# Kernel optimization log

Hardware: AMD Instinct MI355X
Metric: run time of the kernel (lower is better)

Reference implementation:

```python
import jax, jax.numpy as jnp
import numpy as np

N = 50000      # nodes
E = 800000     # edges
H, C = 4, 32   # heads, per-head channels
NF = 513       # n_fft//2 + 1 frequency bins
NMEL = 128
NEG_SLOPE_ATT = 0.2   # GATConv leaky_relu slope
NEG_SLOPE_MLP = 0.01  # F.leaky_relu default


def setup_inputs() -> dict:
    key = jax.random.key(0)
    ks = jax.random.split(key, 12)
    s = 0.05
    return {
        "x": jax.random.normal(ks[0], (N, NF), jnp.float32),
        "edge_index": jax.random.randint(ks[1], (2, E), 0, N, dtype=jnp.int32),
        "fb": jax.random.normal(ks[2], (NF, NMEL), jnp.float32) * s,
        "Wg": jax.random.normal(ks[3], (NMEL, H * C), jnp.float32) * s,
        "bias_g": jnp.zeros((H * C,), jnp.float32),
        "att_src": jax.random.normal(ks[4], (H, C), jnp.float32) * s,
        "att_dst": jax.random.normal(ks[5], (H, C), jnp.float32) * s,
        "W1": jax.random.normal(ks[6], (H * C, 256), jnp.float32) * s,
        "b1": jnp.zeros((256,), jnp.float32),
        "W2": jax.random.normal(ks[7], (256, 128), jnp.float32) * s,
        "b2": jnp.zeros((128,), jnp.float32),
        "W3": jax.random.normal(ks[8], (128, 10), jnp.float32) * s,
        "b3": jnp.zeros((10,), jnp.float32),
    }


def gat_conv(h, src, dst, att_src, att_dst, bias_g):
    # h: [N, H, C]; per-edge attention, segment softmax over dst, scatter-add
    a_s = jnp.einsum('nhc,hc->nh', h, att_src)  # [N, H]
    a_d = jnp.einsum('nhc,hc->nh', h, att_dst)  # [N, H]
    e = jax.nn.leaky_relu(a_s[src] + a_d[dst], NEG_SLOPE_ATT)  # [E', H]
    m = jax.ops.segment_max(e, dst, num_segments=N)            # [N, H]
    ex = jnp.exp(e - m[dst])
    denom = jax.ops.segment_sum(ex, dst, num_segments=N)       # [N, H]
    alpha = ex / denom[dst]                                    # [E', H]
    msg = h[src] * alpha[:, :, None]                           # [E', H, C]
    out = jax.ops.segment_sum(msg, dst, num_segments=N)        # [N, H, C]
    return out.reshape(N, H * C) + bias_g


def reference(x, edge_index, fb, Wg, bias_g, att_src, att_dst, W1, b1, W2, b2, W3, b3):
    # learnable mel filterbank projection: [N, NF] -> [N, NMEL]
    x = x @ fb
    # GATConv linear transform, split into heads
    h = (x @ Wg).reshape(N, H, C)
    # add self loops (PyG GATConv default add_self_loops=True)
    loop = jnp.arange(N, dtype=edge_index.dtype)
    src = jnp.concatenate([edge_index[0], loop])
    dst = jnp.concatenate([edge_index[1], loop])
    x = jax.nn.elu(gat_conv(h, src, dst, att_src, att_dst, bias_g))
    # dropout is identity in eval mode
    x = jax.nn.leaky_relu(x @ W1 + b1, NEG_SLOPE_MLP)
    x = jax.nn.leaky_relu(x @ W2 + b2, NEG_SLOPE_MLP)
    x = jax.nn.leaky_relu(x @ W3 + b3, NEG_SLOPE_MLP)
    return jax.nn.softmax(x, axis=-1)
```

## Files before the change

kernel.cpp:

```cpp
#include <hip/hip_runtime.h>
#include <hip/hip_bf16.h>

#define NN 50000
#define EE 800000
#define NFR 513
#define NMEL 128
#define HC 128

typedef __bf16 bf16x8 __attribute__((ext_vector_type(8)));
typedef float floatx4 __attribute__((ext_vector_type(4)));

struct __attribute__((packed, aligned(4))) u4a { unsigned x, y, z, w; };

__device__ __forceinline__ unsigned short f2b(float f) {
    unsigned u = __float_as_uint(f);
    u = (u + 0x7FFFu + ((u >> 16) & 1u)) >> 16;
    return (unsigned short)u;
}
__device__ __forceinline__ unsigned short f2bu(unsigned u) {
    u = (u + 0x7FFFu + ((u >> 16) & 1u)) >> 16;
    return (unsigned short)u;
}
__device__ __forceinline__ float b2f(unsigned short s) {
    return __uint_as_float(((unsigned)s) << 16);
}
__device__ __forceinline__ float lexp(float a) {
    a = a > 0.f ? a : 0.2f * a;
    return __expf(a);
}

__device__ __forceinline__ float ldf(const float* p, long i) { return p[i]; }
__device__ __forceinline__ void stf(float* p, long i, float v) { p[i] = v; }
__device__ __forceinline__ void stf(__hip_bfloat16* p, long i, float v) {
    ((unsigned short*)p)[i] = f2b(v);
}

#define BM 64
#define BN 64
#define BK 16

template<int EPI, typename TA, typename TB, typename TC>
__global__ __launch_bounds__(256) void gemm_k(const TA* __restrict__ A, const TB* __restrict__ B,
                                              TC* __restrict__ C, int M, int Nn, int K,
                                              const float* __restrict__ bias)
{
    __shared__ float As[BK][BM + 4];
    __shared__ float Bs[BK][BN + 4];
    const int t = threadIdx.x;
    const int row0 = blockIdx.x * BM;
    const int col0 = blockIdx.y * BN;
    const int tc = t & 15, tr = t >> 4;
    float acc[4][4] = {};

    for (int kb = 0; kb < K; kb += BK) {
        #pragma unroll
        for (int i = 0; i < 4; ++i) {
            int idx = i * 256 + t;
            int r = idx >> 4, k = idx & 15;
            int gr = row0 + r, gk = kb + k;
            float v = 0.f;
            if (gr < M && gk < K) v = ldf(A, (long)gr * K + gk);
            As[k][r] = v;
        }
        #pragma unroll
        for (int i = 0; i < 4; ++i) {
            int idx = i * 256 + t;
            int c = idx & 63, k = idx >> 6;
            int gk = kb + k, gc = col0 + c;
            float v = 0.f;
            if (gk < K && gc < Nn) v = ldf(B, (long)gk * Nn + gc);
            Bs[k][c] = v;
        }
        __syncthreads();
        #pragma unroll
        for (int kk = 0; kk < BK; ++kk) {
            float4 av = *reinterpret_cast<const float4*>(&As[kk][tr << 2]);
            float4 bv = *reinterpret_cast<const float4*>(&Bs[kk][tc << 2]);
            float a[4] = {av.x, av.y, av.z, av.w};
            float b[4] = {bv.x, bv.y, bv.z, bv.w};
            #pragma unroll
            for (int i = 0; i < 4; ++i)
                #pragma unroll
                for (int j = 0; j < 4; ++j)
                    acc[i][j] += a[i] * b[j];
        }
        __syncthreads();
    }

    #pragma unroll
    for (int i = 0; i < 4; ++i) {
        int gr = row0 + (tr << 2) + i;
        if (gr >= M) continue;
        #pragma unroll
        for (int j = 0; j < 4; ++j) {
            int gc = col0 + (tc << 2) + j;
            if (gc >= Nn) continue;
            float v = acc[i][j];
            if (EPI == 2) {
                stf(C, (long)gc * 544 + gr, v);
            } else {
                if (EPI == 1) { v += bias[gc]; v = v > 0.f ? v : 0.01f * v; }
                stf(C, (long)gr * Nn + gc, v);
            }
        }
    }
}

__global__ void k_trans(const float* __restrict__ in, __hip_bfloat16* __restrict__ outp,
                        int K, int N, int KP)
{
    int id = blockIdx.x * 256 + threadIdx.x;
    if (id >= N * KP) return;
    int n = id / KP, k = id % KP;
    float v = (k < K) ? in[(long)k * N + n] : 0.f;
    ((unsigned short*)outp)[id] = f2b(v);
}

#define PS 40

template<typename T> struct ARegs;
template<> struct ARegs<float> { unsigned v[8]; };
template<> struct ARegs<__hip_bfloat16> { uint4 v; };

__device__ __forceinline__ void loadA_r(const float* __restrict__ A, ARegs<float>& r, int t,
                                        int row0, int M, int K, int kb)
{
    #pragma unroll
    for (int g = 0; g < 2; ++g) {
        int q = g * 256 + t;
        int row = q >> 3, k4 = (q & 7) * 4;
        int gr = row0 + row, gk = kb + k4;
        unsigned f0 = 0, f1 = 0, f2 = 0, f3 = 0;
        if (gr < M) {
            const float* ap = A + (long)gr * K + gk;
            if (gk + 3 < K) {
                u4a u = *reinterpret_cast<const u4a*>(ap);
                f0 = u.x; f1 = u.y; f2 = u.z; f3 = u.w;
            } else {
                if (gk + 0 < K) f0 = __float_as_uint(ap[0]);
                if (gk + 1 < K) f1 = __float_as_uint(ap[1]);
                if (gk + 2 < K) f2 = __float_as_uint(ap[2]);
            }
        }
        r.v[g * 4 + 0] = f0; r.v[g * 4 + 1] = f1;
        r.v[g * 4 + 2] = f2; r.v[g * 4 + 3] = f3;
    }
}

__device__ __forceinline__ void writeA_r(unsigned short* As, const ARegs<float>& r, int t)
{
    #pragma unroll
    for (int g = 0; g < 2; ++g) {
        int q = g * 256 + t;
        int row = q >> 3, k4 = (q & 7) * 4;
        ushort4 pk;
        pk.x = f2bu(r.v[g * 4 + 0]); pk.y = f2bu(r.v[g * 4 + 1]);
        pk.z = f2bu(r.v[g * 4 + 2]); pk.w = f2bu(r.v[g * 4 + 3]);
        *reinterpret_cast<ushort4*>(&As[row * PS + k4]) = pk;
    }
}

__device__ __forceinline__ void loadA_r(const __hip_bfloat16* __restrict__ A, ARegs<__hip_bfloat16>& r,
                                        int t, int row0, int M, int K, int kb)
{
    int row = t >> 2, k8 = (t & 3) * 8;
    int gr = row0 + row;
    uint4 val = make_uint4(0, 0, 0, 0);
    if (gr < M) val = *reinterpret_cast<const uint4*>(A + (long)gr * K + kb + k8);
    r.v = val;
}

__device__ __forceinline__ void writeA_r(unsigned short* As, const ARegs<__hip_bfloat16>& r, int t)
{
    int row = t >> 2, k8 = (t & 3) * 8;
    *reinterpret_cast<uint4*>(&As[row * PS + k8]) = r.v;
}

__device__ __forceinline__ void loadB_r(const __hip_bfloat16* __restrict__ Bt, uint4* bR, int t,
                                        int col0, int Nn, int KB, int kb)
{
    #pragma unroll
    for (int g = 0; g < 2; ++g) {
        int c = g * 256 + t;
        int row = c >> 2, k8 = (c & 3) * 8;
        int gn = col0 + row;
        uint4 val = make_uint4(0, 0, 0, 0);
        if (gn < Nn) val = *reinterpret_cast<const uint4*>(Bt + (long)gn * KB + kb + k8);
        bR[g] = val;
    }
}

__device__ __forceinline__ void writeB_r(unsigned short* Bs, const uint4* bR, int t)
{
    #pragma unroll
    for (int g = 0; g < 2; ++g) {
        int c = g * 256 + t;
        int row = c >> 2, k8 = (c & 3) * 8;
        *reinterpret_cast<uint4*>(&Bs[row * PS + k8]) = bR[g];
    }
}

template<int EPI, typename TA, typename TC>
__global__ __launch_bounds__(256) void mgemm(const TA* __restrict__ A,
                                             const __hip_bfloat16* __restrict__ Bt,
                                             TC* __restrict__ C,
                                             int M, int Nn, int K, int KB,
                                             const float* __restrict__ bias,
                                             const float* __restrict__ pf1,
                                             const float* __restrict__ pf2,
                                             float* __restrict__ po1,
                                             float* __restrict__ po2)
{
    __shared__ unsigned short As[2][64 * PS];
    __shared__ unsigned short Bs[2][128 * PS];

    const int t = threadIdx.x;
    const int row0 = blockIdx.x * 64;
    const int col0 = blockIdx.y * 128;
    const int wave = t >> 6, lane = t & 63;
    const int wm = (wave >> 1) * 32, wn = (wave & 1) * 64;
    const int lm = lane & 15, kq = lane >> 4;

    floatx4 acc[2][4];
    #pragma unroll
    for (int i = 0; i < 2; ++i)
        #pragma unroll
        for (int j = 0; j < 4; ++j)
            acc[i][j] = 0.f;

    ARegs<TA> aR;
    uint4 bR[2];
    loadA_r(A, aR, t, row0, M, K, 0);
    loadB_r(Bt, bR, t, col0, Nn, KB, 0);

    const int nIter = KB >> 5;
    int b = 0;
    for (int it = 0; it < nIter; ++it) {
        writeA_r(As[b], aR, t);
        writeB_r(Bs[b], bR, t);
        if (it + 1 < nIter) {
            loadA_r(A, aR, t, row0, M, K, (it + 1) * 32);
            loadB_r(Bt, bR, t, col0, Nn, KB, (it + 1) * 32);
        }
        asm volatile("s_waitcnt lgkmcnt(0)" ::: "memory");
        __builtin_amdgcn_s_barrier();
        __builtin_amdgcn_sched_barrier(0);

        bf16x8 af[2], bf[4];
        #pragma unroll
        for (int i = 0; i < 2; ++i)
            af[i] = *reinterpret_cast<const bf16x8*>(&As[b][(wm + i * 16 + lm) * PS + kq * 8]);
        #pragma unroll
        for (int j = 0; j < 4; ++j)
            bf[j] = *reinterpret_cast<const bf16x8*>(&Bs[b][(wn + j * 16 + lm) * PS + kq * 8]);
        #pragma unroll
        for (int i = 0; i < 2; ++i)
            #pragma unroll
            for (int j = 0; j < 4; ++j)
                acc[i][j] = __builtin_amdgcn_mfma_f32_16x16x32_bf16(af[i], bf[j], acc[i][j], 0, 0, 0);
        b ^= 1;
    }

    #pragma unroll
    for (int i = 0; i < 2; ++i) {
        #pragma unroll
        for (int r = 0; r < 4; ++r) {
            int gr = row0 + wm + i * 16 + kq * 4 + r;
            if (gr >= M) continue;
            #pragma unroll
            for (int j = 0; j < 4; ++j) {
                int gc = col0 + wn + j * 16 + lm;
                float v = acc[i][j][r];
                if (EPI == 1) { v += bias[gc]; v = v > 0.f ? v : 0.01f * v; }
                stf(C, (long)gr * Nn + gc, v);
            }
        }
    }

    if (EPI == 4) {
        float wsv[4], wdv[4];
        #pragma unroll
        for (int j = 0; j < 4; ++j) {
            int gc = wn + j * 16 + lm;
            wsv[j] = pf1[gc];
            wdv[j] = pf2[gc];
        }
        #pragma unroll
        for (int i = 0; i < 2; ++i) {
            #pragma unroll
            for (int r = 0; r < 4; ++r) {
                float s0 = acc[i][0][r] * wsv[0] + acc[i][1][r] * wsv[1];
                float s1 = acc[i][2][r] * wsv[2] + acc[i][3][r] * wsv[3];
                float d0 = acc[i][0][r] * wdv[0] + acc[i][1][r] * wdv[1];
                float d1 = acc[i][2][r] * wdv[2] + acc[i][3][r] * wdv[3];
                #pragma unroll
                for (int m = 1; m < 16; m <<= 1) {
                    s0 += __shfl_xor(s0, m); s1 += __shfl_xor(s1, m);
                    d0 += __shfl_xor(d0, m); d1 += __shfl_xor(d1, m);
                }
                if (lm == 0) {
                    int grow = row0 + wm + i * 16 + kq * 4 + r;
                    if (grow < M) {
                        int h0 = wn >> 5;
                        po1[grow * 4 + h0]     = s0;
                        po1[grow * 4 + h0 + 1] = s1;
                        po2[grow * 4 + h0]     = d0;
                        po2[grow * 4 + h0 + 1] = d1;
                    }
                }
            }
        }
    }
}

__global__ __launch_bounds__(256) void k_mlp(const __hip_bfloat16* __restrict__ A,
                                             const __hip_bfloat16* __restrict__ W1t,
                                             const __hip_bfloat16* __restrict__ W2t,
                                             const float* __restrict__ b1,
                                             const float* __restrict__ b2,
                                             const float* __restrict__ W3,
                                             const float* __restrict__ b3,
                                             float* __restrict__ out, int M)
{
    __shared__ unsigned short As[2][64 * PS];
    __shared__ unsigned short Bs[2][128 * PS];
    __shared__ unsigned short x1s[64 * 264];
    __shared__ float w3s[1280];

    const int t = threadIdx.x;
    const int row0 = blockIdx.x * 64;
    const int wave = t >> 6, lane = t & 63;
    const int wm = (wave >> 1) * 32, wn = (wave & 1) * 64;
    const int lm = lane & 15, kq = lane >> 4;

    for (int i = t; i < 1280; i += 256) w3s[i] = W3[i];

    ARegs<__hip_bfloat16> aR;
    uint4 bR[2];

    #pragma unroll 1
    for (int cp = 0; cp < 2; ++cp) {
        floatx4 acc[2][4];
        #pragma unroll
        for (int i = 0; i < 2; ++i)
            #pragma unroll
            for (int j = 0; j < 4; ++j) acc[i][j] = 0.f;

        loadA_r(A, aR, t, row0, M, 128, 0);
        loadB_r(W1t, bR, t, cp * 128, 256, 128, 0);
        int b = 0;
        #pragma unroll 1
        for (int it = 0; it < 4; ++it) {
            writeA_r(As[b], aR, t);
            writeB_r(Bs[b], bR, t);
            if (it + 1 < 4) {
                loadA_r(A, aR, t, row0, M, 128, (it + 1) * 32);
                loadB_r(W1t, bR, t, cp * 128, 256, 128, (it + 1) * 32);
            }
            asm volatile("s_waitcnt lgkmcnt(0)" ::: "memory");
            __builtin_amdgcn_s_barrier();
            __builtin_amdgcn_sched_barrier(0);

            bf16x8 af[2], bf[4];
            #pragma unroll
            for (int i = 0; i < 2; ++i)
                af[i] = *reinterpret_cast<const bf16x8*>(&As[b][(wm + i * 16 + lm) * PS + kq * 8]);
            #pragma unroll
            for (int j = 0; j < 4; ++j)
                bf[j] = *reinterpret_cast<const bf16x8*>(&Bs[b][(wn + j * 16 + lm) * PS + kq * 8]);
            #pragma unroll
            for (int i = 0; i < 2; ++i)
                #pragma unroll
                for (int j = 0; j < 4; ++j)
                    acc[i][j] = __builtin_amdgcn_mfma_f32_16x16x32_bf16(af[i], bf[j], acc[i][j], 0, 0, 0);
            b ^= 1;
        }
        #pragma unroll
        for (int i = 0; i < 2; ++i)
            #pragma unroll
            for (int r = 0; r < 4; ++r) {
                int lrow = wm + i * 16 + kq * 4 + r;
                #pragma unroll
                for (int j = 0; j < 4; ++j) {
                    int gc = cp * 128 + wn + j * 16 + lm;
                    float v = acc[i][j][r] + b1[gc];
                    v = v > 0.f ? v : 0.01f * v;
                    x1s[lrow * 264 + gc] = f2b(v);
                }
            }
    }

    loadB_r(W2t, bR, t, 0, 128, 256, 0);
    __syncthreads();

    floatx4 acc[2][4];
    #pragma unroll
    for (int i = 0; i < 2; ++i)
        #pragma unroll
        for (int j = 0; j < 4; ++j) acc[i][j] = 0.f;

    int b = 0;
    #pragma unroll 1
    for (int it = 0; it < 8; ++it) {
        writeB_r(Bs[b], bR, t);
        if (it + 1 < 8) loadB_r(W2t, bR, t, 0, 128, 256, (it + 1) * 32);
        asm volatile("s_waitcnt lgkmcnt(0)" ::: "memory");
        __builtin_amdgcn_s_barrier();
        __builtin_amdgcn_sched_barrier(0);

        bf16x8 af[2], bf[4];
        #pragma unroll
        for (int i = 0; i < 2; ++i)
            af[i] = *reinterpret_cast<const bf16x8*>(&x1s[(wm + i * 16 + lm) * 264 + it * 32 + kq * 8]);
        #pragma unroll
        for (int j = 0; j < 4; ++j)
            bf[j] = *reinterpret_cast<const bf16x8*>(&Bs[b][(wn + j * 16 + lm) * PS + kq * 8]);
        #pragma unroll
        for (int i = 0; i < 2; ++i)
            #pragma unroll
            for (int j = 0; j < 4; ++j)
                acc[i][j] = __builtin_amdgcn_mfma_f32_16x16x32_bf16(af[i], bf[j], acc[i][j], 0, 0, 0);
        b ^= 1;
    }

    __syncthreads();
    unsigned short* x2s = x1s;
    #pragma unroll
    for (int i = 0; i < 2; ++i)
        #pragma unroll
        for (int r = 0; r < 4; ++r) {
            int lrow = wm + i * 16 + kq * 4 + r;
            #pragma unroll
            for (int j = 0; j < 4; ++j) {
                int gc = wn + j * 16 + lm;
                float v = acc[i][j][r] + b2[gc];
                v = v > 0.f ? v : 0.01f * v;
                x2s[lrow * 130 + gc] = f2b(v);
            }
        }
    __syncthreads();

    if (t < 64) {
        int grow = row0 + t;
        if (grow < M) {
            float l[10];
            #pragma unroll
            for (int j = 0; j < 10; ++j) l[j] = b3[j];
            #pragma unroll 8
            for (int c = 0; c < 128; ++c) {
                float xv = b2f(x2s[t * 130 + c]);
                const float* wr = &w3s[c * 10];
                #pragma unroll
                for (int j = 0; j < 10; ++j) l[j] += xv * wr[j];
            }
            float m = -1e30f;
            #pragma unroll
            for (int j = 0; j < 10; ++j) {
                float v = l[j];
                v = v > 0.f ? v : 0.01f * v;
                l[j] = v;
                m = fmaxf(m, v);
            }
            float sum = 0.f;
            #pragma unroll
            for (int j = 0; j < 10; ++j) { l[j] = __expf(l[j] - m); sum += l[j]; }
            float inv = 1.f / sum;
            #pragma unroll
            for (int j = 0; j < 10; ++j) out[(long)grow * 10 + j] = l[j] * inv;
        }
    }
}

__global__ void k_hist(const int* __restrict__ ei, int* __restrict__ hist)
{
    int e = blockIdx.x * 256 + threadIdx.x;
    if (e < EE) atomicAdd(&hist[ei[EE + e]], 1);
}

__global__ __launch_bounds__(512) void k_scan1(const int* __restrict__ hist, int* __restrict__ start,
                                               int* __restrict__ aux)
{
    __shared__ int sm[512];
    int t = threadIdx.x, i = blockIdx.x * 512 + t;
    int v = (i < NN) ? hist[i] : 0;
    sm[t] = v;
    __syncthreads();
    for (int off = 1; off < 512; off <<= 1) {
        int x = (t >= off) ? sm[t - off] : 0;
        __syncthreads();
        sm[t] += x;
        __syncthreads();
    }
    if (i < NN) start[i] = sm[t] - v;
    if (t == 511) aux[blockIdx.x] = sm[511];
}

__global__ void k_scan2(int* __restrict__ aux, int nb)
{
    int l = threadIdx.x;
    int v0 = (l < nb) ? aux[l] : 0;
    int v1 = (64 + l < nb) ? aux[64 + l] : 0;
    int s0 = v0, s1 = v1;
    for (int off = 1; off < 64; off <<= 1) {
        int u0 = __shfl_up(s0, off);
        int u1 = __shfl_up(s1, off);
        if (l >= off) { s0 += u0; s1 += u1; }
    }
    int tot0 = __shfl(s0, 63);
    if (l < nb) aux[l] = s0 - v0;
    if (64 + l < nb) aux[64 + l] = tot0 + s1 - v1;
}

__global__ __launch_bounds__(512) void k_scan3(int* __restrict__ start, int* __restrict__ cursor,
                                               const int* __restrict__ aux)
{
    int i = blockIdx.x * 512 + threadIdx.x;
    if (i < NN) {
        int v = start[i] + aux[blockIdx.x];
        start[i] = v;
        cursor[i] = v;
    }
    if (i == 0) start[NN] = EE;
}

__global__ void k_fill(const int* __restrict__ ei, int* __restrict__ cursor, int* __restrict__ sorted)
{
    int e = blockIdx.x * 256 + threadIdx.x;
    if (e >= EE) return;
    int s = ei[e], d = ei[EE + e];
    int pos = atomicAdd(&cursor[d], 1);
    sorted[pos] = s;
}

__global__ __launch_bounds__(256) void k_agg(const int* __restrict__ start, const int* __restrict__ sorted,
                                             const float* __restrict__ a_s, const float* __restrict__ a_d,
                                             const __hip_bfloat16* __restrict__ h,
                                             const float* __restrict__ bias_g,
                                             __hip_bfloat16* __restrict__ agg)
{
    int wave = threadIdx.x >> 6;
    int lane = threadIdx.x & 63;
    int d = blockIdx.x * 4 + wave;
    if (d >= NN) return;
    int hh = lane >> 4;
    float ad = a_d[d * 4 + hh];
    int e0 = start[d], e1 = start[d + 1];

    float ex = lexp(a_s[d * 4 + hh] + ad);
    unsigned hv = *reinterpret_cast<const unsigned*>(h + (long)d * HC + 2 * lane);
    float acc0 = ex * __uint_as_float(hv << 16);
    float acc1 = ex * __uint_as_float(hv & 0xffff0000u);
    float dsum = ex;

    int e = e0;
    for (; e + 4 <= e1; e += 4) {
        int s0 = sorted[e + 0], s1 = sorted[e + 1], s2 = sorted[e + 2], s3 = sorted[e + 3];
        float as0 = a_s[s0 * 4 + hh], as1 = a_s[s1 * 4 + hh];
        float as2 = a_s[s2 * 4 + hh], as3 = a_s[s3 * 4 + hh];
        unsigned h0 = *reinterpret_cast<const unsigned*>(h + (long)s0 * HC + 2 * lane);
        unsigned h1 = *reinterpret_cast<const unsigned*>(h + (long)s1 * HC + 2 * lane);
        unsigned h2 = *reinterpret_cast<const unsigned*>(h + (long)s2 * HC + 2 * lane);
        unsigned h3 = *reinterpret_cast<const unsigned*>(h + (long)s3 * HC + 2 * lane);
        float x0 = lexp(as0 + ad), x1 = lexp(as1 + ad), x2 = lexp(as2 + ad), x3 = lexp(as3 + ad);
        acc0 += x0 * __uint_as_float(h0 << 16);
        acc1 += x0 * __uint_as_float(h0 & 0xffff0000u);
        acc0 += x1 * __uint_as_float(h1 << 16);
        acc1 += x1 * __uint_as_float(h1 & 0xffff0000u);
        acc0 += x2 * __uint_as_float(h2 << 16);
        acc1 += x2 * __uint_as_float(h2 & 0xffff0000u);
        acc0 += x3 * __uint_as_float(h3 << 16);
        acc1 += x3 * __uint_as_float(h3 & 0xffff0000u);
        dsum += x0 + x1 + x2 + x3;
    }
    for (; e < e1; ++e) {
        int s = sorted[e];
        float xe = lexp(a_s[s * 4 + hh] + ad);
        unsigned hs = *reinterpret_cast<const unsigned*>(h + (long)s * HC + 2 * lane);
        acc0 += xe * __uint_as_float(hs << 16);
        acc1 += xe * __uint_as_float(hs & 0xffff0000u);
        dsum += xe;
    }

    float inv = 1.f / dsum;
    float2 bg = *reinterpret_cast<const float2*>(bias_g + 2 * lane);
    float v0 = acc0 * inv + bg.x;
    float v1 = acc1 * inv + bg.y;
    v0 = v0 > 0.f ? v0 : expm1f(v0);
    v1 = v1 > 0.f ? v1 : expm1f(v1);
    unsigned pk = (unsigned)f2b(v0) | ((unsigned)f2b(v1) << 16);
    *reinterpret_cast<unsigned*>((unsigned short*)agg + (long)d * HC + 2 * lane) = pk;
}

extern "C" void kernel_launch(void* const* d_in, const int* in_sizes, int n_in,
                              void* d_out, int out_size, void* d_ws, size_t ws_size,
                              hipStream_t stream)
{
    const float* x       = (const float*)d_in[0];
    const int*   ei      = (const int*)d_in[1];
    const float* fb      = (const float*)d_in[2];
    const float* Wg      = (const float*)d_in[3];
    const float* bias_g  = (const float*)d_in[4];
    const float* att_src = (const float*)d_in[5];
    const float* att_dst = (const float*)d_in[6];
    const float* W1      = (const float*)d_in[7];
    const float* b1      = (const float*)d_in[8];
    const float* W2      = (const float*)d_in[9];
    const float* b2      = (const float*)d_in[10];
    const float* W3      = (const float*)d_in[11];
    const float* b3      = (const float*)d_in[12];
    float* out = (float*)d_out;
    float* ws = (float*)d_ws;

    float* a_s = ws + 0;
    float* a_d = ws + 200000;
    __hip_bfloat16* fbWgT = (__hip_bfloat16*)(ws + 400000);
    __hip_bfloat16* W1T   = (__hip_bfloat16*)(ws + 434816);
    __hip_bfloat16* W2T   = (__hip_bfloat16*)(ws + 451200);
    int* hist   = (int*)(ws + 467584);
    int* startA = (int*)(ws + 517584);
    int* aux    = (int*)(ws + 567588);
    int* sorted = (int*)(ws + 567720);
    __hip_bfloat16* hbufB = (__hip_bfloat16*)(ws + 1367720);
    __hip_bfloat16* aggB  = (__hip_bfloat16*)(ws + 4567720);
    int* cursor = hist;
    if (ws_size < (size_t)14167720 * sizeof(float)) return;

    hipMemsetAsync(ws + 400000, 0, (size_t)117584 * sizeof(float), stream);

    gemm_k<2, float, float, __hip_bfloat16><<<dim3(9, 2), 256, 0, stream>>>(fb, Wg, fbWgT, NFR, HC, NMEL, nullptr);
    k_trans<<<128, 256, 0, stream>>>(W1, W1T, 128, 256, 128);
    k_trans<<<128, 256, 0, stream>>>(W2, W2T, 256, 128, 256);

    mgemm<4, float, __hip_bfloat16><<<dim3(782, 1), 256, 0, stream>>>(
        x, fbWgT, hbufB, NN, HC, NFR, 544, nullptr, att_src, att_dst, a_s, a_d);

    k_hist<<<(EE + 255) / 256, 256, 0, stream>>>(ei, hist);
    k_scan1<<<98, 512, 0, stream>>>(hist, startA, aux);
    k_scan2<<<1, 64, 0, stream>>>(aux, 98);
    k_scan3<<<98, 512, 0, stream>>>(startA, cursor, aux);
    k_fill<<<(EE + 255) / 256, 256, 0, stream>>>(ei, cursor, sorted);

    k_agg<<<(NN + 3) / 4, 256, 0, stream>>>(startA, sorted, a_s, a_d, hbufB, bias_g, aggB);

    k_mlp<<<782, 256, 0, stream>>>(aggB, W1T, W2T, b1, b2, W3, b3, out, NN);
}
```

Measured before the change: 400.7 us.

## Fuse graph build and aggregation into one cooperative kernel, merge prep launches

Merges the fb·Wg precompute and the two weight transposes into one prep kernel. It folds the destination histogram into extra blocks of the projection GEMM launch, and replaces the scan, fill and aggregation kernels with a single cooperative kernel that uses grid-wide syncs. The goal is to cut the many small kernel launches and the gaps between them. In exchange it adds four grid barriers, and the aggregation now runs as a grid-stride loop over a fixed 1024-block grid, which may lower latency hiding compared with one block per four nodes.

```diff
diff --git a/kernel.cpp b/kernel.cpp
--- a/kernel.cpp
+++ b/kernel.cpp
@@ -1,5 +1,8 @@
 #include <hip/hip_runtime.h>
 #include <hip/hip_bf16.h>
+#include <hip/hip_cooperative_groups.h>
+
+namespace cg = cooperative_groups;
 
 #define NN 50000
 #define EE 800000
@@ -28,38 +31,43 @@
     a = a > 0.f ? a : 0.2f * a;
     return __expf(a);
 }
-
-__device__ __forceinline__ float ldf(const float* p, long i) { return p[i]; }
-__device__ __forceinline__ void stf(float* p, long i, float v) { p[i] = v; }
 __device__ __forceinline__ void stf(__hip_bfloat16* p, long i, float v) {
     ((unsigned short*)p)[i] = f2b(v);
 }
 
-#define BM 64
-#define BN 64
-#define BK 16
-
-template<int EPI, typename TA, typename TB, typename TC>
-__global__ __launch_bounds__(256) void gemm_k(const TA* __restrict__ A, const TB* __restrict__ B,
-                                              TC* __restrict__ C, int M, int Nn, int K,
-                                              const float* __restrict__ bias)
-{
-    __shared__ float As[BK][BM + 4];
-    __shared__ float Bs[BK][BN + 4];
-    const int t = threadIdx.x;
-    const int row0 = blockIdx.x * BM;
-    const int col0 = blockIdx.y * BN;
+__global__ __launch_bounds__(256) void k_prep(const float* __restrict__ fb, const float* __restrict__ Wg,
+                                              __hip_bfloat16* __restrict__ fbWgT,
+                                              const float* __restrict__ W1, __hip_bfloat16* __restrict__ W1T,
+                                              const float* __restrict__ W2, __hip_bfloat16* __restrict__ W2T)
+{
+    const int b = blockIdx.x, t = threadIdx.x;
+    if (b >= 18) {
+        if (b < 146) {
+            int id = (b - 18) * 256 + t;
+            int n = id >> 7, k = id & 127;
+            ((unsigned short*)W1T)[id] = f2b(W1[(long)k * 256 + n]);
+        } else {
+            int id = (b - 146) * 256 + t;
+            int n = id >> 8, k = id & 255;
+            ((unsigned short*)W2T)[id] = f2b(W2[(long)k * 128 + n]);
+        }
+        return;
+    }
+    __shared__ float As[16][68];
+    __shared__ float Bs[16][68];
+    const int row0 = (b % 9) * 64;
+    const int col0 = (b / 9) * 64;
     const int tc = t & 15, tr = t >> 4;
     float acc[4][4] = {};
 
-    for (int kb = 0; kb < K; kb += BK) {
+    for (int kb = 0; kb < NMEL; kb += 16) {
         #pragma unroll
         for (int i = 0; i < 4; ++i) {
             int idx = i * 256 + t;
             int r = idx >> 4, k = idx & 15;
             int gr = row0 + r, gk = kb + k;
             float v = 0.f;
-            if (gr < M && gk < K) v = ldf(A, (long)gr * K + gk);
+            if (gr < NFR) v = fb[(long)gr * NMEL + gk];
             As[k][r] = v;
         }
         #pragma unroll
@@ -67,53 +75,33 @@
             int idx = i * 256 + t;
             int c = idx & 63, k = idx >> 6;
             int gk = kb + k, gc = col0 + c;
-            float v = 0.f;
-            if (gk < K && gc < Nn) v = ldf(B, (long)gk * Nn + gc);
-            Bs[k][c] = v;
+            Bs[k][c] = Wg[(long)gk * HC + gc];
         }
         __syncthreads();
         #pragma unroll
-        for (int kk = 0; kk < BK; ++kk) {
+        for (int kk = 0; kk < 16; ++kk) {
             float4 av = *reinterpret_cast<const float4*>(&As[kk][tr << 2]);
             float4 bv = *reinterpret_cast<const float4*>(&Bs[kk][tc << 2]);
             float a[4] = {av.x, av.y, av.z, av.w};
-            float b[4] = {bv.x, bv.y, bv.z, bv.w};
+            float bb[4] = {bv.x, bv.y, bv.z, bv.w};
             #pragma unroll
             for (int i = 0; i < 4; ++i)
                 #pragma unroll
                 for (int j = 0; j < 4; ++j)
-                    acc[i][j] += a[i] * b[j];
+                    acc[i][j] += a[i] * bb[j];
         }
         __syncthreads();
     }
-
     #pragma unroll
     for (int i = 0; i < 4; ++i) {
         int gr = row0 + (tr << 2) + i;
-        if (gr >= M) continue;
+        if (gr >= NFR) continue;
         #pragma unroll
         for (int j = 0; j < 4; ++j) {
             int gc = col0 + (tc << 2) + j;
-            if (gc >= Nn) continue;
-            float v = acc[i][j];
-            if (EPI == 2) {
-                stf(C, (long)gc * 544 + gr, v);
-            } else {
-                if (EPI == 1) { v += bias[gc]; v = v > 0.f ? v : 0.01f * v; }
-                stf(C, (long)gr * Nn + gc, v);
-            }
-        }
-    }
-}
-
-__global__ void k_trans(const float* __restrict__ in, __hip_bfloat16* __restrict__ outp,
-                        int K, int N, int KP)
-{
-    int id = blockIdx.x * 256 + threadIdx.x;
-    if (id >= N * KP) return;
-    int n = id / KP, k = id % KP;
-    float v = (k < K) ? in[(long)k * N + n] : 0.f;
-    ((unsigned short*)outp)[id] = f2b(v);
+            ((unsigned short*)fbWgT)[(long)gc * 544 + gr] = f2b(acc[i][j]);
+        }
+    }
 }
 
 #define PS 40
@@ -209,8 +197,16 @@
                                              const float* __restrict__ pf1,
                                              const float* __restrict__ pf2,
                                              float* __restrict__ po1,
-                                             float* __restrict__ po2)
-{
+                                             float* __restrict__ po2,
+                                             const int* __restrict__ ei,
+                                             int* __restrict__ hist)
+{
+    if (EPI == 4 && blockIdx.x >= 782) {
+        int e = (blockIdx.x - 782) * 256 + (int)threadIdx.x;
+        if (e < EE) atomicAdd(&hist[ei[EE + e]], 1);
+        return;
+    }
+
     __shared__ unsigned short As[2][64 * PS];
     __shared__ unsigned short Bs[2][128 * PS];
 
@@ -313,6 +309,125 @@
     }
 }
 
+__global__ __launch_bounds__(256) void k_graph(const int* __restrict__ hist,
+                                               int* __restrict__ start,
+                                               int* __restrict__ cursor,
+                                               int* __restrict__ aux,
+                                               const int* __restrict__ ei,
+                                               int* __restrict__ sorted,
+                                               const float* __restrict__ a_s,
+                                               const float* __restrict__ a_d,
+                                               const __hip_bfloat16* __restrict__ h,
+                                               const float* __restrict__ bias_g,
+                                               __hip_bfloat16* __restrict__ agg)
+{
+    cg::grid_group grid = cg::this_grid();
+    const int t = threadIdx.x, bid = blockIdx.x;
+    const int NCH = (NN + 255) / 256;
+    __shared__ int sm[256];
+
+    if (bid < NCH) {
+        int i = bid * 256 + t;
+        int v = (i < NN) ? hist[i] : 0;
+        sm[t] = v;
+        __syncthreads();
+        for (int off = 1; off < 256; off <<= 1) {
+            int x = (t >= off) ? sm[t - off] : 0;
+            __syncthreads();
+            sm[t] += x;
+            __syncthreads();
+        }
+        if (i < NN) start[i] = sm[t] - v;
+        if (t == 255) aux[bid] = sm[255];
+    }
+    grid.sync();
+
+    if (bid == 0) {
+        int v = (t < NCH) ? aux[t] : 0;
+        sm[t] = v;
+        __syncthreads();
+        for (int off = 1; off < 256; off <<= 1) {
+            int x = (t >= off) ? sm[t - off] : 0;
+            __syncthreads();
+            sm[t] += x;
+            __syncthreads();
+        }
+        if (t < NCH) aux[t] = sm[t] - v;
+    }
+    grid.sync();
+
+    if (bid < NCH) {
+        int i = bid * 256 + t;
+        if (i < NN) {
+            int v = start[i] + aux[bid];
+            start[i] = v;
+            cursor[i] = v;
+        }
+    }
+    if (bid == 0 && t == 0) start[NN] = EE;
+    grid.sync();
+
+    for (int e = bid * 256 + t; e < EE; e += (int)gridDim.x * 256) {
+        int s = ei[e], d = ei[EE + e];
+        int pos = atomicAdd(&cursor[d], 1);
+        sorted[pos] = s;
+    }
+    grid.sync();
+
+    {
+        int wave = t >> 6, lane = t & 63;
+        int hh = lane >> 4;
+        for (int d = bid * 4 + wave; d < NN; d += (int)gridDim.x * 4) {
+            float ad = a_d[d * 4 + hh];
+            int e0 = start[d], e1 = start[d + 1];
+
+            float ex = lexp(a_s[d * 4 + hh] + ad);
+            unsigned hv = *reinterpret_cast<const unsigned*>(h + (long)d * HC + 2 * lane);
+            float acc0 = ex * __uint_as_float(hv << 16);
+            float acc1 = ex * __uint_as_float(hv & 0xffff0000u);
+            float dsum = ex;
+
+            int e = e0;
+            for (; e + 4 <= e1; e += 4) {
+                int s0 = sorted[e + 0], s1 = sorted[e + 1], s2 = sorted[e + 2], s3 = sorted[e + 3];
+                float as0 = a_s[s0 * 4 + hh], as1 = a_s[s1 * 4 + hh];
+                float as2 = a_s[s2 * 4 + hh], as3 = a_s[s3 * 4 + hh];
+                unsigned h0 = *reinterpret_cast<const unsigned*>(h + (long)s0 * HC + 2 * lane);
+                unsigned h1 = *reinterpret_cast<const unsigned*>(h + (long)s1 * HC + 2 * lane);
+                unsigned h2 = *reinterpret_cast<const unsigned*>(h + (long)s2 * HC + 2 * lane);
+                unsigned h3 = *reinterpret_cast<const unsigned*>(h + (long)s3 * HC + 2 * lane);
+                float x0 = lexp(as0 + ad), x1 = lexp(as1 + ad), x2 = lexp(as2 + ad), x3 = lexp(as3 + ad);
+                acc0 += x0 * __uint_as_float(h0 << 16);
+                acc1 += x0 * __uint_as_float(h0 & 0xffff0000u);
+                acc0 += x1 * __uint_as_float(h1 << 16);
+                acc1 += x1 * __uint_as_float(h1 & 0xffff0000u);
+                acc0 += x2 * __uint_as_float(h2 << 16);
+                acc1 += x2 * __uint_as_float(h2 & 0xffff0000u);
+                acc0 += x3 * __uint_as_float(h3 << 16);
+                acc1 += x3 * __uint_as_float(h3 & 0xffff0000u);
+                dsum += x0 + x1 + x2 + x3;
+            }
+            for (; e < e1; ++e) {
+                int s = sorted[e];
+                float xe = lexp(a_s[s * 4 + hh] + ad);
+                unsigned hs = *reinterpret_cast<const unsigned*>(h + (long)s * HC + 2 * lane);
+                acc0 += xe * __uint_as_float(hs << 16);
+                acc1 += xe * __uint_as_float(hs & 0xffff0000u);
+                dsum += xe;
+            }
+
+            float inv = 1.f / dsum;
+            float2 bg = *reinterpret_cast<const float2*>(bias_g + 2 * lane);
+            float v0 = acc0 * inv + bg.x;
+            float v1 = acc1 * inv + bg.y;
+            v0 = v0 > 0.f ? v0 : expm1f(v0);
+            v1 = v1 > 0.f ? v1 : expm1f(v1);
+            unsigned pk = (unsigned)f2b(v0) | ((unsigned)f2b(v1) << 16);
+            *reinterpret_cast<unsigned*>((unsigned short*)agg + (long)d * HC + 2 * lane) = pk;
+        }
+    }
+}
+
 __global__ __launch_bounds__(256) void k_mlp(const __hip_bfloat16* __restrict__ A,
                                              const __hip_bfloat16* __restrict__ W1t,
                                              const __hip_bfloat16* __restrict__ W2t,
@@ -469,126 +584,6 @@
             for (int j = 0; j < 10; ++j) out[(long)grow * 10 + j] = l[j] * inv;
         }
     }
-}
-
-__global__ void k_hist(const int* __restrict__ ei, int* __restrict__ hist)
-{
-    int e = blockIdx.x * 256 + threadIdx.x;
-    if (e < EE) atomicAdd(&hist[ei[EE + e]], 1);
-}
-
-__global__ __launch_bounds__(512) void k_scan1(const int* __restrict__ hist, int* __restrict__ start,
-                                               int* __restrict__ aux)
-{
-    __shared__ int sm[512];
-    int t = threadIdx.x, i = blockIdx.x * 512 + t;
-    int v = (i < NN) ? hist[i] : 0;
-    sm[t] = v;
-    __syncthreads();
-    for (int off = 1; off < 512; off <<= 1) {
-        int x = (t >= off) ? sm[t - off] : 0;
-        __syncthreads();
-        sm[t] += x;
-        __syncthreads();
-    }
-    if (i < NN) start[i] = sm[t] - v;
-    if (t == 511) aux[blockIdx.x] = sm[511];
-}
-
-__global__ void k_scan2(int* __restrict__ aux, int nb)
-{
-    int l = threadIdx.x;
-    int v0 = (l < nb) ? aux[l] : 0;
-    int v1 = (64 + l < nb) ? aux[64 + l] : 0;
-    int s0 = v0, s1 = v1;
-    for (int off = 1; off < 64; off <<= 1) {
-        int u0 = __shfl_up(s0, off);
-        int u1 = __shfl_up(s1, off);
-        if (l >= off) { s0 += u0; s1 += u1; }
-    }
-    int tot0 = __shfl(s0, 63);
-    if (l < nb) aux[l] = s0 - v0;
-    if (64 + l < nb) aux[64 + l] = tot0 + s1 - v1;
-}
-
-__global__ __launch_bounds__(512) void k_scan3(int* __restrict__ start, int* __restrict__ cursor,
-                                               const int* __restrict__ aux)
-{
-    int i = blockIdx.x * 512 + threadIdx.x;
-    if (i < NN) {
-        int v = start[i] + aux[blockIdx.x];
-        start[i] = v;
-        cursor[i] = v;
-    }
-    if (i == 0) start[NN] = EE;
-}
-
-__global__ void k_fill(const int* __restrict__ ei, int* __restrict__ cursor, int* __restrict__ sorted)
-{
-    int e = blockIdx.x * 256 + threadIdx.x;
-    if (e >= EE) return;
-    int s = ei[e], d = ei[EE + e];
-    int pos = atomicAdd(&cursor[d], 1);
-    sorted[pos] = s;
-}
-
-__global__ __launch_bounds__(256) void k_agg(const int* __restrict__ start, const int* __restrict__ sorted,
-                                             const float* __restrict__ a_s, const float* __restrict__ a_d,
-                                             const __hip_bfloat16* __restrict__ h,
-                                             const float* __restrict__ bias_g,
-                                             __hip_bfloat16* __restrict__ agg)
-{
-    int wave = threadIdx.x >> 6;
-    int lane = threadIdx.x & 63;
-    int d = blockIdx.x * 4 + wave;
-    if (d >= NN) return;
-    int hh = lane >> 4;
-    float ad = a_d[d * 4 + hh];
-    int e0 = start[d], e1 = start[d + 1];
-
-    float ex = lexp(a_s[d * 4 + hh] + ad);
-    unsigned hv = *reinterpret_cast<const unsigned*>(h + (long)d * HC + 2 * lane);
-    float acc0 = ex * __uint_as_float(hv << 16);
-    float acc1 = ex * __uint_as_float(hv & 0xffff0000u);
-    float dsum = ex;
-
-    int e = e0;
-    for (; e + 4 <= e1; e += 4) {
-        int s0 = sorted[e + 0], s1 = sorted[e + 1], s2 = sorted[e + 2], s3 = sorted[e + 3];
-        float as0 = a_s[s0 * 4 + hh], as1 = a_s[s1 * 4 + hh];
-        float as2 = a_s[s2 * 4 + hh], as3 = a_s[s3 * 4 + hh];
-        unsigned h0 = *reinterpret_cast<const unsigned*>(h + (long)s0 * HC + 2 * lane);
-        unsigned h1 = *reinterpret_cast<const unsigned*>(h + (long)s1 * HC + 2 * lane);
-        unsigned h2 = *reinterpret_cast<const unsigned*>(h + (long)s2 * HC + 2 * lane);
-        unsigned h3 = *reinterpret_cast<const unsigned*>(h + (long)s3 * HC + 2 * lane);
-        float x0 = lexp(as0 + ad), x1 = lexp(as1 + ad), x2 = lexp(as2 + ad), x3 = lexp(as3 + ad);
-        acc0 += x0 * __uint_as_float(h0 << 16);
-        acc1 += x0 * __uint_as_float(h0 & 0xffff0000u);
-        acc0 += x1 * __uint_as_float(h1 << 16);
-        acc1 += x1 * __uint_as_float(h1 & 0xffff0000u);
-        acc0 += x2 * __uint_as_float(h2 << 16);
-        acc1 += x2 * __uint_as_float(h2 & 0xffff0000u);
-        acc0 += x3 * __uint_as_float(h3 << 16);
-        acc1 += x3 * __uint_as_float(h3 & 0xffff0000u);
-        dsum += x0 + x1 + x2 + x3;
-    }
-    for (; e < e1; ++e) {
-        int s = sorted[e];
-        float xe = lexp(a_s[s * 4 + hh] + ad);
-        unsigned hs = *reinterpret_cast<const unsigned*>(h + (long)s * HC + 2 * lane);
-        acc0 += xe * __uint_as_float(hs << 16);
-        acc1 += xe * __uint_as_float(hs & 0xffff0000u);
-        dsum += xe;
-    }
-
-    float inv = 1.f / dsum;
-    float2 bg = *reinterpret_cast<const float2*>(bias_g + 2 * lane);
-    float v0 = acc0 * inv + bg.x;
-    float v1 = acc1 * inv + bg.y;
-    v0 = v0 > 0.f ? v0 : expm1f(v0);
-    v1 = v1 > 0.f ? v1 : expm1f(v1);
-    unsigned pk = (unsigned)f2b(v0) | ((unsigned)f2b(v1) << 16);
-    *reinterpret_cast<unsigned*>((unsigned short*)agg + (long)d * HC + 2 * lane) = pk;
 }
 
 extern "C" void kernel_launch(void* const* d_in, const int* in_sizes, int n_in,
@@ -618,29 +613,26 @@
     __hip_bfloat16* W2T   = (__hip_bfloat16*)(ws + 451200);
     int* hist   = (int*)(ws + 467584);
     int* startA = (int*)(ws + 517584);
-    int* aux    = (int*)(ws + 567588);
     int* sorted = (int*)(ws + 567720);
     __hip_bfloat16* hbufB = (__hip_bfloat16*)(ws + 1367720);
     __hip_bfloat16* aggB  = (__hip_bfloat16*)(ws + 4567720);
+    int* aux    = (int*)(ws + 7767720);
     int* cursor = hist;
     if (ws_size < (size_t)14167720 * sizeof(float)) return;
 
     hipMemsetAsync(ws + 400000, 0, (size_t)117584 * sizeof(float), stream);
 
-    gemm_k<2, float, float, __hip_bfloat16><<<dim3(9, 2), 256, 0, stream>>>(fb, Wg, fbWgT, NFR, HC, NMEL, nullptr);
-    k_trans<<<128, 256, 0, stream>>>(W1, W1T, 128, 256, 128);
-    k_trans<<<128, 256, 0, stream>>>(W2, W2T, 256, 128, 256);
-
-    mgemm<4, float, __hip_bfloat16><<<dim3(782, 1), 256, 0, stream>>>(
-        x, fbWgT, hbufB, NN, HC, NFR, 544, nullptr, att_src, att_dst, a_s, a_d);
-
-    k_hist<<<(EE + 255) / 256, 256, 0, stream>>>(ei, hist);
-    k_scan1<<<98, 512, 0, stream>>>(hist, startA, aux);
-    k_scan2<<<1, 64, 0, stream>>>(aux, 98);
-    k_scan3<<<98, 512, 0, stream>>>(startA, cursor, aux);
-    k_fill<<<(EE + 255) / 256, 256, 0, stream>>>(ei, cursor, sorted);
-
-    k_agg<<<(NN + 3) / 4, 256, 0, stream>>>(startA, sorted, a_s, a_d, hbufB, bias_g, aggB);
+    k_prep<<<274, 256, 0, stream>>>(fb, Wg, fbWgT, W1, W1T, W2, W2T);
+
+    mgemm<4, float, __hip_bfloat16><<<dim3(782 + (EE + 255) / 256, 1), 256, 0, stream>>>(
+        x, fbWgT, hbufB, NN, HC, NFR, 544, nullptr, att_src, att_dst, a_s, a_d, ei, hist);
+
+    {
+        void* kArgs[] = { (void*)&hist, (void*)&startA, (void*)&cursor, (void*)&aux,
+                          (void*)&ei, (void*)&sorted, (void*)&a_s, (void*)&a_d,
+                          (void*)&hbufB, (void*)&bias_g, (void*)&aggB };
+        hipLaunchCooperativeKernel((void*)k_graph, dim3(1024), dim3(256), kArgs, 0, stream);
+    }
 
     k_mlp<<<782, 256, 0, stream>>>(aggB, W1T, W2T, b1, b2, W3, b3, out, NN);
 }
```

After: 856.4 us. +113.7%, slower.
